# Kernel optimization log

Hardware: AMD Instinct MI355X
Metric: run time of the kernel (lower is better)

The kernel has to match this reference:

```python
import jax, jax.numpy as jnp
import numpy as np

B, N, DIM, H, DH = 16, 1024, 768, 12, 64
SCALE = DH ** -0.5


def setup_inputs() -> dict:
    key = jax.random.key(0)
    k1, k2, k3 = jax.random.split(key, 3)
    x = jax.random.normal(k1, (B, N, DIM), dtype=jnp.float32)
    W_qkv = jax.random.normal(k2, (DIM, 3 * H * DH), dtype=jnp.float32) * (DIM ** -0.5)
    W_out = jax.random.normal(k3, (H * DH, DIM), dtype=jnp.float32) * ((H * DH) ** -0.5)
    b_out = jnp.zeros((DIM,), dtype=jnp.float32)
    # perm = [0] + random shuffle of 1..N-1 (matches module's construction)
    rng = np.random.default_rng(0)
    perm = jnp.asarray(np.concatenate([[0], rng.permutation(np.arange(1, N))]), dtype=jnp.int32)
    return {"x": x, "W_qkv": W_qkv, "W_out": W_out, "b_out": b_out, "perm": perm}


def reference(x, W_qkv, W_out, b_out, perm):
    # QKV projection: [b, n, 3*h*d]
    qkv = jnp.einsum('bnd,de->bne', x, W_qkv)
    q, k, v = jnp.split(qkv, 3, axis=-1)
    # [b, n, h*d] -> [b, h, n, d]
    reshape = lambda t: t.reshape(B, N, H, DH).transpose(0, 2, 1, 3)
    q, k, v = reshape(q), reshape(k), reshape(v)
    # permute query rows
    q = q[:, :, perm]
    dots = jnp.einsum('bhqd,bhkd->bhqk', q, k) * SCALE
    attn = jax.nn.softmax(dots, axis=-1)
    out = jnp.einsum('bhqk,bhkd->bhqd', attn, v)
    out = out.transpose(0, 2, 1, 3).reshape(B, N, H * DH)
    return jnp.einsum('bne,ed->bnd', out, W_out) + b_out
```

## Files before the change

kernel.cpp:

```cpp
#include <hip/hip_runtime.h>
#include <hip/hip_bf16.h>


typedef __bf16 bf16x8 __attribute__((ext_vector_type(8)));
typedef __bf16 bf16x4 __attribute__((ext_vector_type(4)));
typedef float  f32x4  __attribute__((ext_vector_type(4)));

__device__ __forceinline__ f32x4 mfma16(bf16x8 a, bf16x8 b, f32x4 c) {
    return __builtin_amdgcn_mfma_f32_16x16x32_bf16(a, b, c, 0, 0, 0);
}

__device__ __forceinline__ void async16(const void* g, void* l) {
    __builtin_amdgcn_global_load_lds(
        (const __attribute__((address_space(1))) unsigned int*)g,
        (__attribute__((address_space(3))) unsigned int*)l,
        16, 0, 0);
}

__global__ void detect_dtype(const unsigned short* __restrict__ raw, int* __restrict__ flag) {
    __shared__ int cnt;
    if (threadIdx.x == 0) cnt = 0;
    __syncthreads();
    int local = 0;
    for (int i = threadIdx.x; i < 2048; i += 256) {
        unsigned e = (raw[i] >> 7) & 0xFFu;
        if (e >= 0xC0u) local++;
    }
    atomicAdd(&cnt, local);
    __syncthreads();
    if (threadIdx.x == 0) *flag = (cnt > 16) ? 1 : 0;
}

__global__ void convert_to_bf16(const void* __restrict__ src, __bf16* __restrict__ dst,
                                int n4, const int* __restrict__ flag) {
    const int f = *flag;
    int i = blockIdx.x * blockDim.x + threadIdx.x;
    const int stride = gridDim.x * blockDim.x;
    if (f) {
        const float4* s = (const float4*)src;
        for (; i < n4; i += stride) {
            float4 v = s[i];
            bf16x4 o;
            o[0] = (__bf16)v.x; o[1] = (__bf16)v.y;
            o[2] = (__bf16)v.z; o[3] = (__bf16)v.w;
            *(bf16x4*)&dst[(size_t)i * 4] = o;
        }
    } else {
        const ushort4* s = (const ushort4*)src;
        for (; i < n4; i += stride) *(ushort4*)&dst[(size_t)i * 4] = s[i];
    }
}

__global__ void transpose_dyn(const void* __restrict__ in, __bf16* __restrict__ out,
                              int R, int C, const int* __restrict__ flag) {
    __shared__ __bf16 tile[64][65];
    const int f = *flag;
    const int c0 = blockIdx.x * 64, r0 = blockIdx.y * 64;
    const int tx = threadIdx.x, ty = threadIdx.y;
#pragma unroll
    for (int k = 0; k < 16; ++k) {
        int r = ty + 4 * k;
        size_t idx = (size_t)(r0 + r) * C + c0 + tx;
        tile[r][tx] = f ? (__bf16)((const float*)in)[idx] : ((const __bf16*)in)[idx];
    }
    __syncthreads();
#pragma unroll
    for (int k = 0; k < 16; ++k) {
        int cc = ty + 4 * k;
        out[(size_t)(c0 + cc) * R + r0 + tx] = tile[tx][cc];
    }
}

#define GMFMA16()                                                       \
    acc[0][0] = mfma16(af0, bf0, acc[0][0]);                            \
    acc[0][1] = mfma16(af0, bf1, acc[0][1]);                            \
    acc[0][2] = mfma16(af0, bf2, acc[0][2]);                            \
    acc[0][3] = mfma16(af0, bf3, acc[0][3]);                            \
    acc[1][0] = mfma16(af1, bf0, acc[1][0]);                            \
    acc[1][1] = mfma16(af1, bf1, acc[1][1]);                            \
    acc[1][2] = mfma16(af1, bf2, acc[1][2]);                            \
    acc[1][3] = mfma16(af1, bf3, acc[1][3]);                            \
    acc[2][0] = mfma16(af2, bf0, acc[2][0]);                            \
    acc[2][1] = mfma16(af2, bf1, acc[2][1]);                            \
    acc[2][2] = mfma16(af2, bf2, acc[2][2]);                            \
    acc[2][3] = mfma16(af2, bf3, acc[2][3]);                            \
    acc[3][0] = mfma16(af3, bf0, acc[3][0]);                            \
    acc[3][1] = mfma16(af3, bf1, acc[3][1]);                            \
    acc[3][2] = mfma16(af3, bf2, acc[3][2]);                            \
    acc[3][3] = mfma16(af3, bf3, acc[3][3])

#define GTILE(RD, ST, DO_STAGE, VMK) do {                               \
    if ((VMK) == 4)                                                     \
        asm volatile("s_waitcnt vmcnt(4) lgkmcnt(0)" ::: "memory");     \
    else                                                                \
        asm volatile("s_waitcnt vmcnt(0) lgkmcnt(0)" ::: "memory");     \
    __builtin_amdgcn_s_barrier();                                       \
    if (DO_STAGE) {                                                     \
        async16(gA0, smem + (ST) + stA0);                               \
        async16(gA1, smem + (ST) + stA1);                               \
        async16(gB0, smem + (ST) + 8192 + stA0);                        \
        async16(gB1, smem + (ST) + 8192 + stA1);                        \
        gA0 += 32; gA1 += 32; gB0 += 32; gB1 += 32;                     \
    }                                                                   \
    bf16x8 af0 = *(const bf16x8*)(smem + (RD) + aoff0);                 \
    bf16x8 af1 = *(const bf16x8*)(smem + (RD) + aoff1);                 \
    bf16x8 af2 = *(const bf16x8*)(smem + (RD) + aoff2);                 \
    bf16x8 af3 = *(const bf16x8*)(smem + (RD) + aoff3);                 \
    bf16x8 bf0 = *(const bf16x8*)(smem + (RD) + boff0);                 \
    bf16x8 bf1 = *(const bf16x8*)(smem + (RD) + boff1);                 \
    bf16x8 bf2 = *(const bf16x8*)(smem + (RD) + boff2);                 \
    bf16x8 bf3 = *(const bf16x8*)(smem + (RD) + boff3);                 \
    GMFMA16();                                                          \
} while (0)

template <int MODE>
__global__ __launch_bounds__(256, 3)
void gemm_bt(const __bf16* __restrict__ A, int lda,
             const __bf16* __restrict__ Bt,
             const void* __restrict__ bias,
             void* __restrict__ Cout, int ldc,
             int K, const int* __restrict__ flag,
             __bf16* __restrict__ vt) {
    __shared__ __align__(16) char smem[49152];
    const int tid  = threadIdx.x;
    const int wid  = tid >> 6;
    const int lane = tid & 63;
    const int quad = lane >> 4;
    const int l15  = lane & 15;

    const int bm = blockIdx.x * 128;
    const int bn = blockIdx.y * 128;

    const int wm = (wid & 1) * 64;
    const int wn = (wid >> 1) * 64;
    const int srow  = lane >> 2;
    const int sslot = lane & 3;

    const int rA0 = wid * 16 + srow;
    const int rA1 = 64 + wid * 16 + srow;
    const __bf16* gA0 = A  + (size_t)(bm + rA0) * lda + ((sslot ^ ((rA0 >> 1) & 3)) << 3);
    const __bf16* gA1 = A  + (size_t)(bm + rA1) * lda + ((sslot ^ ((rA1 >> 1) & 3)) << 3);
    const __bf16* gB0 = Bt + (size_t)(bn + rA0) * K   + ((sslot ^ ((rA0 >> 1) & 3)) << 3);
    const __bf16* gB1 = Bt + (size_t)(bn + rA1) * K   + ((sslot ^ ((rA1 >> 1) & 3)) << 3);
    const int stA0 = (wid * 16) * 64;
    const int stA1 = (64 + wid * 16) * 64;

    const int rf0 = wm + 0 * 16 + l15, rf1 = wm + 1 * 16 + l15;
    const int rf2 = wm + 2 * 16 + l15, rf3 = wm + 3 * 16 + l15;
    const int aoff0 = rf0 * 64 + ((quad ^ ((rf0 >> 1) & 3)) * 16);
    const int aoff1 = rf1 * 64 + ((quad ^ ((rf1 >> 1) & 3)) * 16);
    const int aoff2 = rf2 * 64 + ((quad ^ ((rf2 >> 1) & 3)) * 16);
    const int aoff3 = rf3 * 64 + ((quad ^ ((rf3 >> 1) & 3)) * 16);
    const int rg0 = wn + 0 * 16 + l15, rg1 = wn + 1 * 16 + l15;
    const int rg2 = wn + 2 * 16 + l15, rg3 = wn + 3 * 16 + l15;
    const int boff0 = 8192 + rg0 * 64 + ((quad ^ ((rg0 >> 1) & 3)) * 16);
    const int boff1 = 8192 + rg1 * 64 + ((quad ^ ((rg1 >> 1) & 3)) * 16);
    const int boff2 = 8192 + rg2 * 64 + ((quad ^ ((rg2 >> 1) & 3)) * 16);
    const int boff3 = 8192 + rg3 * 64 + ((quad ^ ((rg3 >> 1) & 3)) * 16);

    f32x4 acc[4][4];
#pragma unroll
    for (int i = 0; i < 4; ++i)
#pragma unroll
        for (int j = 0; j < 4; ++j) acc[i][j] = (f32x4)0.0f;

    async16(gA0, smem + stA0);
    async16(gA1, smem + stA1);
    async16(gB0, smem + 8192 + stA0);
    async16(gB1, smem + 8192 + stA1);
    gA0 += 32; gA1 += 32; gB0 += 32; gB1 += 32;
    async16(gA0, smem + 16384 + stA0);
    async16(gA1, smem + 16384 + stA1);
    async16(gB0, smem + 16384 + 8192 + stA0);
    async16(gB1, smem + 16384 + 8192 + stA1);
    gA0 += 32; gA1 += 32; gB0 += 32; gB1 += 32;

#pragma unroll 1
    for (int g = 0; g < 7; ++g) {
        GTILE(0,     32768, true, 4);
        GTILE(16384, 0,     true, 4);
        GTILE(32768, 16384, true, 4);
    }
    GTILE(0,     32768, true,  4);
    GTILE(16384, 0,     false, 4);
    GTILE(32768, 0,     false, 0);

    if (MODE == 0 && bn >= 1536) {
        const int bq = bm >> 10;
        const int n0 = (bm & 1023) + wm + quad * 4;
        const int colb = bn - 1536 + wn;
#pragma unroll
        for (int mi = 0; mi < 4; ++mi)
#pragma unroll
            for (int ni = 0; ni < 4; ++ni) {
                int col = colb + ni * 16 + l15;
                bf16x4 v;
                v[0] = (__bf16)acc[mi][ni][0];
                v[1] = (__bf16)acc[mi][ni][1];
                v[2] = (__bf16)acc[mi][ni][2];
                v[3] = (__bf16)acc[mi][ni][3];
                *(bf16x4*)&vt[((size_t)bq * 768 + col) * 1024 + n0 + mi * 16] = v;
            }
        return;
    }

    const int f = (MODE == 1) ? *flag : 0;
    if (MODE == 1) {
#pragma unroll
        for (int ni = 0; ni < 4; ++ni) {
            int col = bn + wn + ni * 16 + l15;
            float bv = f ? ((const float*)bias)[col] : (float)((const __bf16*)bias)[col];
#pragma unroll
            for (int mi = 0; mi < 4; ++mi)
#pragma unroll
                for (int rg = 0; rg < 4; ++rg) acc[mi][ni][rg] += bv;
        }
    }

    if (MODE == 0 || !f) {
        __bf16* cs = (__bf16*)smem;
#pragma unroll
        for (int c = 0; c < 4; ++c) {
            __syncthreads();
            if (wm == (c >> 1) * 64) {
                int mb = (c & 1) * 2;
#pragma unroll
                for (int mloc = 0; mloc < 2; ++mloc) {
                    int rowc = mloc * 16 + quad * 4;
#pragma unroll
                    for (int ni = 0; ni < 4; ++ni) {
                        int col = wn + ni * 16 + l15;
#pragma unroll
                        for (int rg = 0; rg < 4; ++rg)
                            cs[(rowc + rg) * 136 + col] = (__bf16)acc[mb + mloc][ni][rg];
                    }
                }
            }
            __syncthreads();
#pragma unroll
            for (int p = 0; p < 2; ++p) {
                int row  = p * 16 + (tid >> 4);
                int colc = tid & 15;
                bf16x8 v = *(const bf16x8*)&cs[row * 136 + colc * 8];
                *(bf16x8*)((__bf16*)Cout + (size_t)(bm + c * 32 + row) * ldc + bn + colc * 8) = v;
            }
        }
    } else {
        float* cs = (float*)smem;
#pragma unroll
        for (int c = 0; c < 8; ++c) {
            __syncthreads();
            if (wm == (c >> 2) * 64) {
                int mi = c & 3;
                int rowc = quad * 4;
#pragma unroll
                for (int ni = 0; ni < 4; ++ni) {
                    int col = wn + ni * 16 + l15;
#pragma unroll
                    for (int rg = 0; rg < 4; ++rg)
                        cs[(rowc + rg) * 132 + col] = acc[mi][ni][rg];
                }
            }
            __syncthreads();
#pragma unroll
            for (int p = 0; p < 2; ++p) {
                int row  = p * 8 + (tid >> 5);
                int colc = tid & 31;
                float4 v = *(const float4*)&cs[row * 132 + colc * 4];
                *(float4*)((float*)Cout + (size_t)(bm + c * 16 + row) * ldc + bn + colc * 4) = v;
            }
        }
    }
}

__global__ __launch_bounds__(256, 2)
void attn(const __bf16* qkv, const __bf16* __restrict__ vt,
          const int* __restrict__ perm, __bf16* O, int ldo) {
    __shared__ __align__(16) char smem[55296];
    __bf16* Qs = (__bf16*)smem;
    __bf16* Ps = (__bf16*)(smem + 32768);

    const int tid  = threadIdx.x;
    const int wid  = tid >> 6;
    const int lane = tid & 63;
    const int quad = lane >> 4;
    const int l15  = lane & 15;
    const int bh = blockIdx.x;
    const int q0 = blockIdx.y * 128;
    const int b = bh / 12, h = bh % 12;
    const size_t row_base = (size_t)b * 1024;
    const int qcol = h * 64;
    const int kcol = 768 + h * 64;
    const int srow8  = lane >> 3;
    const int sslot8 = lane & 7;
    __bf16* Pw = Ps + wid * (32 * 88);

#pragma unroll
    for (int is = 0; is < 4; ++is) {
        int r = is * 32 + wid * 8 + srow8;
        int gr = perm[q0 + r];
        int chunk = sslot8 ^ (r & 7);
        async16(qkv + (row_base + gr) * 2304 + qcol + chunk * 8,
                &Qs[(is * 32 + wid * 8) * 64]);
    }
    __syncthreads();

    bf16x8 qf[2][2];
#pragma unroll
    for (int mi = 0; mi < 2; ++mi) {
        int r = wid * 32 + mi * 16 + l15;
#pragma unroll
        for (int ks = 0; ks < 2; ++ks)
            qf[mi][ks] = *(const bf16x8*)&Qs[r * 64 + (((ks * 4 + quad) ^ (r & 7)) * 8)];
    }
    asm volatile("s_waitcnt lgkmcnt(0)" ::: "memory");
    __builtin_amdgcn_sched_barrier(0);
    __builtin_amdgcn_s_barrier();

    const int off0 = l15 * 64 + (((0 * 4 + quad) ^ (l15 & 7)) * 8);
    const int off1 = l15 * 64 + (((1 * 4 + quad) ^ (l15 & 7)) * 8);
    const int pwb  = l15 * 88 + quad * 4;
    const int pfb  = l15 * 88 + quad * 8;

    const int rK = wid * 8 + srow8;
    const int ck = sslot8 ^ (rK & 7);
    const __bf16* kg0 = qkv + (row_base + rK) * 2304 + kcol + ck * 8;
    const __bf16* kg1 = kg0 + (size_t)32 * 2304;
    const __bf16* vg0 = vt + ((size_t)bh * 64 + rK) * 1024 + ck * 8;
    const __bf16* vg1 = vg0 + (size_t)32 * 1024;

    f32x4 acco[2][4];
#pragma unroll
    for (int mi = 0; mi < 2; ++mi)
#pragma unroll
        for (int ni = 0; ni < 4; ++ni) acco[mi][ni] = (f32x4)0.0f;
    float lsum[2] = {0.0f, 0.0f};

    const float cfac = 0.125f * 1.44269504088896340736f;

#define ASTAGE(KB, VB) do {                                             \
        async16(kg0, smem + (KB) + wid * 1024);                         \
        async16(kg1, smem + (KB) + 4096 + wid * 1024);                  \
        async16(vg0, smem + (VB) + wid * 1024);                         \
        async16(vg1, smem + (VB) + 4096 + wid * 1024);                  \
        kg0 += (size_t)64 * 2304; kg1 += (size_t)64 * 2304;             \
        vg0 += 64; vg1 += 64;                                           \
    } while (0)

    auto compute = [&](const __bf16* Kb, const __bf16* Vb) {
#pragma unroll
        for (int half = 0; half < 2; ++half) {
            f32x4 accs[2][2];
#pragma unroll
            for (int ki = 0; ki < 2; ++ki)
#pragma unroll
                for (int mi = 0; mi < 2; ++mi) accs[ki][mi] = (f32x4)0.0f;
#pragma unroll
            for (int ks = 0; ks < 2; ++ks) {
                const int off = ks ? off1 : off0;
                bf16x8 kf0 = *(const bf16x8*)&Kb[(half * 2 + 0) * 1024 + off];
                bf16x8 kf1 = *(const bf16x8*)&Kb[(half * 2 + 1) * 1024 + off];
                accs[0][0] = mfma16(kf0, qf[0][ks], accs[0][0]);
                accs[0][1] = mfma16(kf0, qf[1][ks], accs[0][1]);
                accs[1][0] = mfma16(kf1, qf[0][ks], accs[1][0]);
                accs[1][1] = mfma16(kf1, qf[1][ks], accs[1][1]);
            }

#pragma unroll
            for (int ki = 0; ki < 2; ++ki)
#pragma unroll
                for (int mi = 0; mi < 2; ++mi) {
                    bf16x4 pk;
                    float s0 = __builtin_amdgcn_exp2f(accs[ki][mi][0] * cfac - 8.0f);
                    float s1 = __builtin_amdgcn_exp2f(accs[ki][mi][1] * cfac - 8.0f);
                    float s2 = __builtin_amdgcn_exp2f(accs[ki][mi][2] * cfac - 8.0f);
                    float s3 = __builtin_amdgcn_exp2f(accs[ki][mi][3] * cfac - 8.0f);
                    pk[0] = (__bf16)s0; pk[1] = (__bf16)s1;
                    pk[2] = (__bf16)s2; pk[3] = (__bf16)s3;
                    lsum[mi] += (s0 + s1) + (s2 + s3);
                    *(bf16x4*)&Pw[pwb + mi * 1408 + (half * 2 + ki) * 16] = pk;
                }

            {
                bf16x8 pf0 = *(const bf16x8*)&Pw[pfb + 0 * 1408 + half * 32];
                bf16x8 pf1 = *(const bf16x8*)&Pw[pfb + 1 * 1408 + half * 32];
                const int offv = half ? off1 : off0;
#pragma unroll
                for (int ni = 0; ni < 4; ++ni) {
                    bf16x8 vf = *(const bf16x8*)&Vb[ni * 1024 + offv];
                    acco[0][ni] = mfma16(pf0, vf, acco[0][ni]);
                    acco[1][ni] = mfma16(pf1, vf, acco[1][ni]);
                }
            }
        }
    };

    ASTAGE(0, 16384);

#pragma unroll 1
    for (int kt2 = 0; kt2 < 8; ++kt2) {
        asm volatile("s_waitcnt vmcnt(0) lgkmcnt(0)" ::: "memory");
        __builtin_amdgcn_s_barrier();
        ASTAGE(8192, 16384 + 8192);
        compute((const __bf16*)smem, (const __bf16*)(smem + 16384));
        asm volatile("s_waitcnt vmcnt(0) lgkmcnt(0)" ::: "memory");
        __builtin_amdgcn_s_barrier();
        if (kt2 < 7) ASTAGE(0, 16384);
        compute((const __bf16*)(smem + 8192), (const __bf16*)(smem + 16384 + 8192));
    }
#undef ASTAGE

#pragma unroll
    for (int off = 16; off < 64; off <<= 1) {
        lsum[0] += __shfl_xor(lsum[0], off, 64);
        lsum[1] += __shfl_xor(lsum[1], off, 64);
    }

#pragma unroll
    for (int mi = 0; mi < 2; ++mi) {
#pragma unroll
        for (int rg = 0; rg < 4; ++rg) {
            float inv = 1.0f / __shfl(lsum[mi], quad * 4 + rg, 64);
            int orow = q0 + wid * 32 + mi * 16 + quad * 4 + rg;
#pragma unroll
            for (int ni = 0; ni < 4; ++ni) {
                int ocol = h * 64 + ni * 16 + l15;
                O[(row_base + orow) * (size_t)ldo + ocol] = (__bf16)(acco[mi][ni][rg] * inv);
            }
        }
    }
}

extern "C" void kernel_launch(void* const* d_in, const int* in_sizes, int n_in,
                              void* d_out, int out_size, void* d_ws, size_t ws_size,
                              hipStream_t stream) {
    (void)in_sizes; (void)n_in; (void)out_size; (void)ws_size;
    const void* x_raw    = d_in[0];
    const void* Wqkv_raw = d_in[1];
    const void* Wout_raw = d_in[2];
    const void* bout_raw = d_in[3];
    const int*  perm     = (const int*)d_in[4];

    char* ws = (char*)d_ws;
    int*    flag = (int*)ws;
    __bf16* Xc   = (__bf16*)(ws + 256);
    __bf16* QKV  = (__bf16*)(ws + 25166080);
    __bf16* Vt   = (__bf16*)(ws + 100663552);
    __bf16* Wqt  = (__bf16*)(ws + 125829376);
    __bf16* Wot  = (__bf16*)(ws + 129368320);
    __bf16* Obuf = QKV + 1536;

    detect_dtype<<<1, 256, 0, stream>>>((const unsigned short*)x_raw, flag);
    convert_to_bf16<<<2048, 256, 0, stream>>>(x_raw, Xc, 16384 * 768 / 4, flag);
    transpose_dyn<<<dim3(36, 12), dim3(64, 4), 0, stream>>>(Wqkv_raw, Wqt, 768, 2304, flag);
    transpose_dyn<<<dim3(12, 12), dim3(64, 4), 0, stream>>>(Wout_raw, Wot, 768, 768, flag);
    gemm_bt<0><<<dim3(128, 18), 256, 0, stream>>>(Xc, 768, Wqt, nullptr, QKV, 2304, 768, nullptr, Vt);
    attn<<<dim3(192, 8), 256, 0, stream>>>(QKV, Vt, perm, Obuf, 2304);
    gemm_bt<1><<<dim3(128, 6), 256, 0, stream>>>(Obuf, 2304, Wot, bout_raw, d_out, 768, 768, flag, nullptr);
}
```

Baseline: 206.5 us.

## Fuse dtype detection, conversion and weight transposes into one prep kernel; swap GEMM grid order

Merges the dtype-detect, input conversion and two weight-transpose kernels into a single launch. Each block redundantly samples its own input to compute the dtype flag, which removes three launches and the serial dependency on the detect kernel. The GEMM grids are also reordered so that consecutive blocks walk the N dimension first, which should improve L2 reuse of the A tile. The cost is the redundant flag sampling in every block and a more complex block-dispatch prologue.

```diff
diff --git a/kernel.cpp b/kernel.cpp
--- a/kernel.cpp
+++ b/kernel.cpp
@@ -17,57 +17,75 @@
         16, 0, 0);
 }
 
-__global__ void detect_dtype(const unsigned short* __restrict__ raw, int* __restrict__ flag) {
+__global__ __launch_bounds__(256)
+void prep(const void* __restrict__ x, __bf16* __restrict__ Xc,
+          const void* __restrict__ Wqkv, __bf16* __restrict__ Wqt,
+          const void* __restrict__ Wout, __bf16* __restrict__ Wot,
+          int* __restrict__ flag) {
+    __shared__ __bf16 tile[64][65];
     __shared__ int cnt;
-    if (threadIdx.x == 0) cnt = 0;
+    const int bid = blockIdx.x;
+    const int tid = threadIdx.x;
+
+    const unsigned short* raw =
+        (bid < 1024) ? (const unsigned short*)x
+                     : (bid < 1456) ? (const unsigned short*)Wqkv
+                                    : (const unsigned short*)Wout;
+    if (tid == 0) cnt = 0;
     __syncthreads();
     int local = 0;
-    for (int i = threadIdx.x; i < 2048; i += 256) {
+    for (int i = tid; i < 2048; i += 256) {
         unsigned e = (raw[i] >> 7) & 0xFFu;
         if (e >= 0xC0u) local++;
     }
     atomicAdd(&cnt, local);
     __syncthreads();
-    if (threadIdx.x == 0) *flag = (cnt > 16) ? 1 : 0;
-}
-
-__global__ void convert_to_bf16(const void* __restrict__ src, __bf16* __restrict__ dst,
-                                int n4, const int* __restrict__ flag) {
-    const int f = *flag;
-    int i = blockIdx.x * blockDim.x + threadIdx.x;
-    const int stride = gridDim.x * blockDim.x;
-    if (f) {
-        const float4* s = (const float4*)src;
-        for (; i < n4; i += stride) {
-            float4 v = s[i];
-            bf16x4 o;
-            o[0] = (__bf16)v.x; o[1] = (__bf16)v.y;
-            o[2] = (__bf16)v.z; o[3] = (__bf16)v.w;
-            *(bf16x4*)&dst[(size_t)i * 4] = o;
+    const int f = (cnt > 16) ? 1 : 0;
+    if (bid == 0 && tid == 0) *flag = f;
+
+    if (bid < 1024) {
+        const int n4 = 16384 * 768 / 4;
+        int i = bid * 256 + tid;
+        const int stride = 1024 * 256;
+        if (f) {
+            const float4* s = (const float4*)x;
+            for (; i < n4; i += stride) {
+                float4 v = s[i];
+                bf16x4 o;
+                o[0] = (__bf16)v.x; o[1] = (__bf16)v.y;
+                o[2] = (__bf16)v.z; o[3] = (__bf16)v.w;
+                *(bf16x4*)&Xc[(size_t)i * 4] = o;
+            }
+        } else {
+            const ushort4* s = (const ushort4*)x;
+            for (; i < n4; i += stride) *(ushort4*)&Xc[(size_t)i * 4] = s[i];
         }
     } else {
-        const ushort4* s = (const ushort4*)src;
-        for (; i < n4; i += stride) *(ushort4*)&dst[(size_t)i * 4] = s[i];
-    }
-}
-
-__global__ void transpose_dyn(const void* __restrict__ in, __bf16* __restrict__ out,
-                              int R, int C, const int* __restrict__ flag) {
-    __shared__ __bf16 tile[64][65];
-    const int f = *flag;
-    const int c0 = blockIdx.x * 64, r0 = blockIdx.y * 64;
-    const int tx = threadIdx.x, ty = threadIdx.y;
-#pragma unroll
-    for (int k = 0; k < 16; ++k) {
-        int r = ty + 4 * k;
-        size_t idx = (size_t)(r0 + r) * C + c0 + tx;
-        tile[r][tx] = f ? (__bf16)((const float*)in)[idx] : ((const __bf16*)in)[idx];
-    }
-    __syncthreads();
-#pragma unroll
-    for (int k = 0; k < 16; ++k) {
-        int cc = ty + 4 * k;
-        out[(size_t)(c0 + cc) * R + r0 + tx] = tile[tx][cc];
+        const void* in;
+        __bf16* out;
+        int R, C, c0, r0;
+        if (bid < 1456) {
+            int t = bid - 1024;
+            in = Wqkv; out = Wqt; R = 768; C = 2304;
+            c0 = (t % 36) * 64; r0 = (t / 36) * 64;
+        } else {
+            int t = bid - 1456;
+            in = Wout; out = Wot; R = 768; C = 768;
+            c0 = (t % 12) * 64; r0 = (t / 12) * 64;
+        }
+        const int tx = tid & 63, ty = tid >> 6;
+#pragma unroll
+        for (int k = 0; k < 16; ++k) {
+            int r = ty + 4 * k;
+            size_t idx = (size_t)(r0 + r) * C + c0 + tx;
+            tile[r][tx] = f ? (__bf16)((const float*)in)[idx] : ((const __bf16*)in)[idx];
+        }
+        __syncthreads();
+#pragma unroll
+        for (int k = 0; k < 16; ++k) {
+            int cc = ty + 4 * k;
+            out[(size_t)(c0 + cc) * R + r0 + tx] = tile[tx][cc];
+        }
     }
 }
 
@@ -128,8 +146,8 @@
     const int quad = lane >> 4;
     const int l15  = lane & 15;
 
-    const int bm = blockIdx.x * 128;
-    const int bn = blockIdx.y * 128;
+    const int bm = blockIdx.y * 128;
+    const int bn = blockIdx.x * 128;
 
     const int wm = (wid & 1) * 64;
     const int wn = (wid >> 1) * 64;
@@ -450,11 +468,8 @@
     __bf16* Wot  = (__bf16*)(ws + 129368320);
     __bf16* Obuf = QKV + 1536;
 
-    detect_dtype<<<1, 256, 0, stream>>>((const unsigned short*)x_raw, flag);
-    convert_to_bf16<<<2048, 256, 0, stream>>>(x_raw, Xc, 16384 * 768 / 4, flag);
-    transpose_dyn<<<dim3(36, 12), dim3(64, 4), 0, stream>>>(Wqkv_raw, Wqt, 768, 2304, flag);
-    transpose_dyn<<<dim3(12, 12), dim3(64, 4), 0, stream>>>(Wout_raw, Wot, 768, 768, flag);
-    gemm_bt<0><<<dim3(128, 18), 256, 0, stream>>>(Xc, 768, Wqt, nullptr, QKV, 2304, 768, nullptr, Vt);
+    prep<<<1600, 256, 0, stream>>>(x_raw, Xc, Wqkv_raw, Wqt, Wout_raw, Wot, flag);
+    gemm_bt<0><<<dim3(18, 128), 256, 0, stream>>>(Xc, 768, Wqt, nullptr, QKV, 2304, 768, nullptr, Vt);
     attn<<<dim3(192, 8), 256, 0, stream>>>(QKV, Vt, perm, Obuf, 2304);
-    gemm_bt<1><<<dim3(128, 6), 256, 0, stream>>>(Obuf, 2304, Wot, bout_raw, d_out, 768, 768, flag, nullptr);
-}
+    gemm_bt<1><<<dim3(6, 128), 256, 0, stream>>>(Obuf, 2304, Wot, bout_raw, d_out, 768, 768, flag, nullptr);
+}
```

Result: no change. 206.6 us (+0.1%).
